# Performance work log

Hardware: AMD Instinct MI355X
Metric: run time of the kernel (lower is better)

Reference implementation:

```python
import jax, jax.numpy as jnp
import numpy as np


def setup_inputs() -> dict:
    key = jax.random.key(0)
    k1, k2, k3 = jax.random.split(key, 3)
    B, Lc, Lq, D = 32, 1024, 128, 1024
    context_features = jax.random.normal(k1, (B, Lc, D), dtype=jnp.float32)
    question_features = jax.random.normal(k2, (B, Lq, D), dtype=jnp.float32)
    # weight of nn.Linear(3*D, 1, bias=False): shape (3*D,), split into w1,w2,w3
    w = jax.random.normal(k3, (3 * D,), dtype=jnp.float32) * (1.0 / np.sqrt(3 * D))
    return {"context_features": context_features, "question_features": question_features, "w": w}


def reference(context_features, question_features, w):
    B, Lc, D = context_features.shape
    Lq = question_features.shape[1]
    w1, w2, w3 = w[:D], w[D:2 * D], w[2 * D:]
    # Trilinear similarity: sim[b,i,j] = w1.c_i + w2.q_j + w3.(c_i*q_j)
    # Decomposed so the (B,Lc,Lq,3D) concat tensor is never materialized.
    sim = (
        jnp.einsum("bcd,d->bc", context_features, w1)[:, :, None]      # [B,Lc,1]
        + jnp.einsum("bqd,d->bq", question_features, w2)[:, None, :]    # [B,1,Lq]
        + jnp.einsum("bcd,bqd->bcq", context_features * w3, question_features)
    )  # [B,Lc,Lq]
    # context-to-question attention
    c2q = jnp.einsum("bcq,bqd->bcd", jax.nn.softmax(sim, axis=2), question_features)
    # question-to-context attention
    b = jax.nn.softmax(jnp.max(sim, axis=2), axis=-1)                   # [B,Lc]
    q2c = jnp.einsum("bc,bcd->bd", b, context_features)                 # [B,D]
    q2c = jnp.broadcast_to(q2c[:, None, :], (B, Lc, D))                 # repeat over Lc
    return (c2q, q2c)
```

## Files before the change

kernel.cpp:

```cpp
#include <hip/hip_runtime.h>
#include <hip/hip_bf16.h>
#include <stdint.h>

#define B_  32
#define LC  1024
#define LQ  128
#define DD  1024
#define CT  64
#define BK  64

typedef __attribute__((ext_vector_type(8))) short short8;
typedef __attribute__((ext_vector_type(4))) float f4;
typedef unsigned short u16;

__device__ __forceinline__ u16 f2bf(float f) {
  __hip_bfloat16 h = __float2bfloat16(f);
  return *reinterpret_cast<u16*>(&h);
}

__device__ __forceinline__ void gld16(const u16* g, void* l) {
  __builtin_amdgcn_global_load_lds(
      (const __attribute__((address_space(1))) unsigned int*)g,
      (__attribute__((address_space(3))) unsigned int*)l,
      16, 0, 0);
}

__global__ __launch_bounds__(256) void k1m(const float* __restrict__ qf,
                                           const float* __restrict__ w,
                                           u16* __restrict__ qw3_bf,
                                           u16* __restrict__ qT_bf,
                                           float* __restrict__ qwpart) {
  __shared__ float w3s[128];
  __shared__ float w2s[128];
  __shared__ __align__(16) u16 ldsq[128][136];
  int blk = blockIdx.x;
  int b = blk >> 3, dt = blk & 7;
  int t = threadIdx.x;
  if (t < 128) { w3s[t] = w[2 * DD + dt * 128 + t]; w2s[t] = w[DD + dt * 128 + t]; }
  __syncthreads();
  {
    int q = t >> 1, half = t & 1;
    const float* src = qf + (size_t)(b * LQ + q) * DD + dt * 128 + half * 64;
    u16* dst = qw3_bf + (size_t)(b * LQ + q) * DD + dt * 128 + half * 64;
    float s2 = 0.f;
    #pragma unroll
    for (int j = 0; j < 8; ++j) {
      float4 a = *(const float4*)(src + j * 8);
      float4 c = *(const float4*)(src + j * 8 + 4);
      float vals[8] = {a.x, a.y, a.z, a.w, c.x, c.y, c.z, c.w};
      u16 u3[8] __attribute__((aligned(16)));
      #pragma unroll
      for (int jj = 0; jj < 8; ++jj) {
        int dl = half * 64 + j * 8 + jj;
        s2 += vals[jj] * w2s[dl];
        u3[jj] = f2bf(vals[jj] * w3s[dl]);
        ldsq[dl][q] = f2bf(vals[jj]);
      }
      *(short8*)(dst + j * 8) = *(short8*)u3;
    }
    s2 += __shfl_xor(s2, 1);
    if (half == 0) qwpart[(size_t)(b * 8 + dt) * LQ + q] = s2;
  }
  __syncthreads();
  {
    int d = t >> 1, qh = (t & 1) * 64;
    u16* gdst = qT_bf + (size_t)b * DD * LQ + (size_t)(dt * 128 + d) * LQ + qh;
    #pragma unroll
    for (int i = 0; i < 8; ++i) {
      short8 v = *(const short8*)(&ldsq[d][qh + i * 8]);
      *(short8*)(gdst + i * 8) = v;
    }
  }
}

__device__ __forceinline__ void stage3(const u16* aqT, int dt,
                                       unsigned char* qbase, int wv, int lane) {
  #pragma unroll
  for (int i = 0; i < 4; ++i) {
    unsigned rel = wv * 4096 + i * 1024 + lane * 16;
    int r = rel >> 8, c = (rel >> 4) & 15, cs = c ^ (r & 7);
    gld16(aqT + (size_t)(dt * 64 + r) * LQ + cs * 8, qbase + wv * 4096 + i * 1024);
  }
}

__global__ __launch_bounds__(256, 3) void kA(const float* __restrict__ ctx,
                                          const u16* __restrict__ qw3_bf,
                                          const u16* __restrict__ qT_bf,
                                          const float* __restrict__ w,
                                          const float* __restrict__ qwpart,
                                          float* __restrict__ c2q,
                                          float* __restrict__ partial,
                                          float* __restrict__ tileM,
                                          float* __restrict__ tileS) {
  __shared__ __align__(16) unsigned char tile[49152];
  __shared__ float cws[CT];
  __shared__ float qws[LQ];
  __shared__ float rm2[2][CT];
  __shared__ float rs2[2][CT];
  __shared__ float rmax[CT];
  __shared__ float rinv[CT];
  __shared__ float wgtl[CT];

  unsigned char* psm = tile + 32768;

  const int tid = threadIdx.x;
  const int bid = blockIdx.x;
  const int blk = (bid & 7) * 64 + (bid >> 3);
  const int b   = blk >> 4;
  const int c0  = (blk & 15) * CT;
  const int lane = tid & 63;
  const int wv   = tid >> 6;
  const int wr   = wv >> 1;
  const int wc   = wv & 1;
  const int l15  = lane & 15;
  const int l4   = lane >> 4;

  if (tid < LQ) {
    float s = 0.f;
    #pragma unroll
    for (int dt = 0; dt < 8; ++dt) s += qwpart[(size_t)(b * 8 + dt) * LQ + tid];
    qws[tid] = s;
  }

  f4 acc[2][4];
  #pragma unroll
  for (int m = 0; m < 2; ++m)
    #pragma unroll
    for (int n = 0; n < 4; ++n) { f4 z = {0.f, 0.f, 0.f, 0.f}; acc[m][n] = z; }

  const float* actx = ctx + (size_t)(b * LC + c0) * DD;
  const u16* aq3  = qw3_bf + (size_t)b * LQ * DD;
  const u16* aqT  = qT_bf + (size_t)b * DD * LQ;

  const int ar  = tid >> 2;
  const int akc = (tid & 3) * 16;

  float va[16];
  float cwp = 0.f;
  const float* w1p = w + akc;

  {
    const float* s = actx + (size_t)ar * DD + akc;
    *(float4*)(va)      = *(const float4*)(s);
    *(float4*)(va + 4)  = *(const float4*)(s + 4);
    *(float4*)(va + 8)  = *(const float4*)(s + 8);
    *(float4*)(va + 12) = *(const float4*)(s + 12);
    #pragma unroll
    for (int i = 0; i < 4; ++i) {
      unsigned rel = wv * 4096 + i * 1024 + lane * 16;
      int r = rel >> 7, c = (rel >> 4) & 7, cs = c ^ (r & 7);
      gld16(aq3 + (size_t)r * DD + cs * 8, tile + 8192 + wv * 4096 + i * 1024);
    }
    #pragma unroll
    for (int j = 0; j < 4; ++j) {
      float4 wv4 = *(const float4*)(w1p + j * 4);
      cwp += va[j * 4 + 0] * wv4.x + va[j * 4 + 1] * wv4.y +
             va[j * 4 + 2] * wv4.z + va[j * 4 + 3] * wv4.w;
    }
    u16 u[16] __attribute__((aligned(16)));
    #pragma unroll
    for (int j = 0; j < 16; ++j) u[j] = f2bf(va[j]);
    int cu = akc >> 3;
    *(short8*)(tile + ar * 128 + ((cu ^ (ar & 7)) << 4))       = *(short8*)u;
    *(short8*)(tile + ar * 128 + (((cu + 1) ^ (ar & 7)) << 4)) = *(short8*)(u + 8);
  }
  __syncthreads();

  for (int t = 0; t < 16; ++t) {
    int cur = t & 1;
    unsigned char* bufc = tile + cur * 24576;
    unsigned char* bufn = tile + (cur ^ 1) * 24576;
    if (t < 15) {
      int k0_ = (t + 1) * BK;
      const float* s = actx + (size_t)ar * DD + k0_ + akc;
      *(float4*)(va)      = *(const float4*)(s);
      *(float4*)(va + 4)  = *(const float4*)(s + 4);
      *(float4*)(va + 8)  = *(const float4*)(s + 8);
      *(float4*)(va + 12) = *(const float4*)(s + 12);
      #pragma unroll
      for (int i = 0; i < 4; ++i) {
        unsigned rel = wv * 4096 + i * 1024 + lane * 16;
        int r = rel >> 7, c = (rel >> 4) & 7, cs = c ^ (r & 7);
        gld16(aq3 + (size_t)r * DD + k0_ + cs * 8, bufn + 8192 + wv * 4096 + i * 1024);
      }
      #pragma unroll
      for (int j = 0; j < 4; ++j) {
        float4 wv4 = *(const float4*)(w1p + k0_ + j * 4);
        cwp += va[j * 4 + 0] * wv4.x + va[j * 4 + 1] * wv4.y +
               va[j * 4 + 2] * wv4.z + va[j * 4 + 3] * wv4.w;
      }
    }
    #pragma unroll
    for (int kk = 0; kk < 2; ++kk) {
      short8 afr[2], bfr[4];
      #pragma unroll
      for (int m = 0; m < 2; ++m) {
        int r = wr * 32 + m * 16 + l15;
        int byte = r * 128 + kk * 64 + l4 * 16;
        byte ^= (r & 7) << 4;
        afr[m] = *(const short8*)(bufc + byte);
      }
      #pragma unroll
      for (int n = 0; n < 4; ++n) {
        int r = wc * 64 + n * 16 + l15;
        int byte = r * 128 + kk * 64 + l4 * 16;
        byte ^= (r & 7) << 4;
        bfr[n] = *(const short8*)(bufc + 8192 + byte);
      }
      #pragma unroll
      for (int m = 0; m < 2; ++m)
        #pragma unroll
        for (int n = 0; n < 4; ++n)
          acc[m][n] = __builtin_amdgcn_mfma_f32_16x16x32_bf16(afr[m], bfr[n], acc[m][n], 0, 0, 0);
    }
    if (t < 15) {
      u16 u[16] __attribute__((aligned(16)));
      #pragma unroll
      for (int j = 0; j < 16; ++j) u[j] = f2bf(va[j]);
      int cu = akc >> 3;
      *(short8*)(bufn + ar * 128 + ((cu ^ (ar & 7)) << 4))       = *(short8*)u;
      *(short8*)(bufn + ar * 128 + (((cu + 1) ^ (ar & 7)) << 4)) = *(short8*)(u + 8);
    }
    __syncthreads();
  }

  cwp += __shfl_xor(cwp, 1);
  cwp += __shfl_xor(cwp, 2);
  if ((lane & 3) == 0) cws[ar] = cwp;
  __syncthreads();

  #pragma unroll
  for (int m = 0; m < 2; ++m) {
    #pragma unroll
    for (int j = 0; j < 4; ++j) {
      int cl = wr * 32 + m * 16 + l4 * 4 + j;
      float mx = -1e30f;
      #pragma unroll
      for (int n = 0; n < 4; ++n) {
        float v = acc[m][n][j] + cws[cl] + qws[wc * 64 + n * 16 + l15];
        acc[m][n][j] = v;
        mx = fmaxf(mx, v);
      }
      #pragma unroll
      for (int off = 1; off < 16; off <<= 1) mx = fmaxf(mx, __shfl_xor(mx, off));
      if (l15 == 0) rm2[wc][cl] = mx;
    }
  }
  __syncthreads();
  if (tid < CT) rmax[tid] = fmaxf(rm2[0][tid], rm2[1][tid]);
  __syncthreads();
  #pragma unroll
  for (int m = 0; m < 2; ++m) {
    #pragma unroll
    for (int j = 0; j < 4; ++j) {
      int cl = wr * 32 + m * 16 + l4 * 4 + j;
      float mx = rmax[cl];
      float s = 0.f;
      #pragma unroll
      for (int n = 0; n < 4; ++n) {
        float p = __expf(acc[m][n][j] - mx);
        s += p;
        int q = wc * 64 + n * 16 + l15;
        int byte = cl * (LQ * 2) + q * 2;
        byte ^= (cl & 7) << 4;
        *(u16*)(psm + byte) = f2bf(p);
      }
      #pragma unroll
      for (int off = 1; off < 16; off <<= 1) s += __shfl_xor(s, off);
      if (l15 == 0) rs2[wc][cl] = s;
    }
  }
  __syncthreads();
  if (tid < CT) {
    rinv[tid] = 1.f / (rs2[0][tid] + rs2[1][tid]);
    float m = rmax[tid];
    float M = m;
    #pragma unroll
    for (int off = 32; off; off >>= 1) M = fmaxf(M, __shfl_xor(M, off));
    float wq = __expf(m - M);
    wgtl[tid] = wq;
    float S = wq;
    #pragma unroll
    for (int off = 32; off; off >>= 1) S += __shfl_xor(S, off);
    if (tid == 0) { tileM[blk] = M; tileS[blk] = S; }
  }
  __syncthreads();

  stage3(aqT, 0, tile, wv, lane);
  __syncthreads();

  float ri[2];
  ri[0] = rinv[wr * 32 + l15];
  ri[1] = rinv[wr * 32 + 16 + l15];

  f4 pacc25 = {0.f, 0.f, 0.f, 0.f};
  const float* pbase = actx + tid * 4;

  for (int dt = 0; dt < 16; ++dt) {
    int cur = dt & 1;
    if (dt < 15) stage3(aqT, dt + 1, tile + (cur ^ 1) * 16384, wv, lane);
    #pragma unroll
    for (int cc = 0; cc < 4; ++cc) {
      int c = dt * 4 + cc;
      pacc25 += wgtl[c] * *(const f4*)(pbase + (size_t)c * DD);
    }
    unsigned char* qbase = tile + cur * 16384;
    f4 pacc[2][2];
    #pragma unroll
    for (int n = 0; n < 2; ++n)
      #pragma unroll
      for (int m = 0; m < 2; ++m) { f4 z = {0.f, 0.f, 0.f, 0.f}; pacc[n][m] = z; }
    #pragma unroll
    for (int kk = 0; kk < 4; ++kk) {
      short8 pa[2], qb[2];
      #pragma unroll
      for (int m = 0; m < 2; ++m) {
        int r = wr * 32 + m * 16 + l15;
        int byte = r * 256 + kk * 64 + l4 * 16;
        byte ^= (r & 7) << 4;
        pa[m] = *(const short8*)(psm + byte);
      }
      #pragma unroll
      for (int n = 0; n < 2; ++n) {
        int dl = wc * 32 + n * 16 + l15;
        int byte = dl * 256 + kk * 64 + l4 * 16;
        byte ^= (dl & 7) << 4;
        qb[n] = *(const short8*)(qbase + byte);
      }
      #pragma unroll
      for (int n = 0; n < 2; ++n)
        #pragma unroll
        for (int m = 0; m < 2; ++m)
          pacc[n][m] = __builtin_amdgcn_mfma_f32_16x16x32_bf16(qb[n], pa[m], pacc[n][m], 0, 0, 0);
    }
    #pragma unroll
    for (int n = 0; n < 2; ++n)
      #pragma unroll
      for (int m = 0; m < 2; ++m) {
        f4 v = pacc[n][m] * ri[m];
        int cl = wr * 32 + m * 16 + l15;
        int dc = wc * 32 + n * 16 + l4 * 4;
        *(f4*)(c2q + (size_t)(b * LC + c0 + cl) * DD + dt * 64 + dc) = v;
      }
    __syncthreads();
  }

  *(f4*)(partial + (size_t)blk * DD + tid * 4) = pacc25;
}

__global__ __launch_bounds__(256) void kQC2(const float* __restrict__ partial,
                                            const float* __restrict__ tileM,
                                            const float* __restrict__ tileS,
                                            float* __restrict__ out2) {
  int blk = blockIdx.x;
  int b = blk >> 5, cb = blk & 31;
  int t = threadIdx.x;
  __shared__ float sc[16];
  __shared__ float dninv;
  if (t < 16) {
    float m = tileM[b * 16 + t];
    float M = m;
    #pragma unroll
    for (int off = 8; off; off >>= 1) M = fmaxf(M, __shfl_xor(M, off));
    float e = __expf(m - M);
    sc[t] = e;
    float d = e * tileS[b * 16 + t];
    #pragma unroll
    for (int off = 8; off; off >>= 1) d += __shfl_xor(d, off);
    if (t == 0) dninv = 1.f / d;
  }
  __syncthreads();
  f4 a = {0.f, 0.f, 0.f, 0.f};
  #pragma unroll
  for (int i = 0; i < 16; ++i) {
    float s = sc[i];
    f4 v = *(const f4*)(partial + (size_t)(b * 16 + i) * DD + t * 4);
    a += s * v;
  }
  a *= dninv;
  float* dst = out2 + ((size_t)b * LC + cb * 32) * DD + t * 4;
  #pragma unroll
  for (int r = 0; r < 32; ++r) *(f4*)(dst + (size_t)r * DD) = a;
}

extern "C" void kernel_launch(void* const* d_in, const int* in_sizes, int n_in,
                              void* d_out, int out_size, void* d_ws, size_t ws_size,
                              hipStream_t stream) {
  (void)in_sizes; (void)n_in; (void)out_size; (void)ws_size;
  const float* ctx = (const float*)d_in[0];
  const float* qf  = (const float*)d_in[1];
  const float* w   = (const float*)d_in[2];
  float* out      = (float*)d_out;
  float* c2q      = out;
  float* q2c_out  = out + (size_t)B_ * LC * DD;

  float* ws     = (float*)d_ws;
  float* qwpart = ws;
  float* tileM  = qwpart + B_ * 8 * LQ;
  float* tileS  = tileM + 512;
  float* part   = tileS + 512;
  u16*   qw3_bf = (u16*)(part + 512 * DD);
  u16*   qT_bf  = qw3_bf + (size_t)B_ * LQ * DD;

  hipLaunchKernelGGL(k1m,  dim3(256),  dim3(256), 0, stream, qf, w, qw3_bf, qT_bf, qwpart);
  hipLaunchKernelGGL(kA,   dim3(512),  dim3(256), 0, stream, ctx, qw3_bf, qT_bf, w, qwpart, c2q, part, tileM, tileS);
  hipLaunchKernelGGL(kQC2, dim3(1024), dim3(256), 0, stream, part, tileM, tileS, q2c_out);
}
```

Measured before the change: 137.6 us.

## Deepen context prefetch to two stages with partial vmcnt barriers in kA

Restructures the phase-1 GEMM loop in kA so context rows are register-prefetched two K-steps ahead, using alternating register buffers. Each step now ends with a custom barrier that waits only until vmcnt drops to 4, so the most recent global loads can stay in flight across the barrier. The w1 vector is staged into shared memory instead of being read from global on every step. Launch bounds drop from 3 to 2 blocks per SM, which allows more registers per thread for the second buffer but lowers occupancy. The hand-set vmcnt count is fragile if the compiler reorders or merges loads.

```diff
diff --git a/kernel.cpp b/kernel.cpp
--- a/kernel.cpp
+++ b/kernel.cpp
@@ -23,6 +23,13 @@
       (const __attribute__((address_space(1))) unsigned int*)g,
       (__attribute__((address_space(3))) unsigned int*)l,
       16, 0, 0);
+}
+
+__device__ __forceinline__ void barrier_vm4() {
+  __builtin_amdgcn_sched_barrier(0);
+  asm volatile("s_waitcnt vmcnt(4) lgkmcnt(0)" ::: "memory");
+  __builtin_amdgcn_s_barrier();
+  __builtin_amdgcn_sched_barrier(0);
 }
 
 __global__ __launch_bounds__(256) void k1m(const float* __restrict__ qf,
@@ -83,7 +90,84 @@
   }
 }
 
-__global__ __launch_bounds__(256, 3) void kA(const float* __restrict__ ctx,
+#define STAGEB_PH1(K0, BUF)                                                    \
+  do {                                                                         \
+    _Pragma("unroll")                                                          \
+    for (int i_ = 0; i_ < 4; ++i_) {                                           \
+      unsigned rel_ = wv * 4096 + i_ * 1024 + lane * 16;                       \
+      int r_ = rel_ >> 7, c_ = (rel_ >> 4) & 7, cs_ = c_ ^ (r_ & 7);           \
+      gld16(aq3 + (size_t)r_ * DD + (K0) + cs_ * 8,                            \
+            (BUF) + 8192 + wv * 4096 + i_ * 1024);                             \
+    }                                                                          \
+  } while (0)
+
+#define LOADCTX_PH1(VA, K0)                                                    \
+  do {                                                                         \
+    const float* s_ = actx + (size_t)ar * DD + (K0) + akc;                     \
+    *(float4*)(VA)      = *(const float4*)(s_);                                \
+    *(float4*)(VA + 4)  = *(const float4*)(s_ + 4);                            \
+    *(float4*)(VA + 8)  = *(const float4*)(s_ + 8);                            \
+    *(float4*)(VA + 12) = *(const float4*)(s_ + 12);                           \
+  } while (0)
+
+#define CWWRITE_PH1(VA, K0, BUF)                                               \
+  do {                                                                         \
+    _Pragma("unroll")                                                          \
+    for (int j_ = 0; j_ < 4; ++j_) {                                           \
+      float4 w4_ = *(const float4*)(&w1s[(K0) + akc + j_ * 4]);                \
+      cwp += (VA)[j_ * 4 + 0] * w4_.x + (VA)[j_ * 4 + 1] * w4_.y +             \
+             (VA)[j_ * 4 + 2] * w4_.z + (VA)[j_ * 4 + 3] * w4_.w;              \
+    }                                                                          \
+    {                                                                          \
+      u16 u_[16] __attribute__((aligned(16)));                                 \
+      _Pragma("unroll")                                                        \
+      for (int j_ = 0; j_ < 16; ++j_) u_[j_] = f2bf((VA)[j_]);                 \
+      int cu_ = akc >> 3;                                                      \
+      *(short8*)((BUF) + ar * 128 + ((cu_ ^ (ar & 7)) << 4)) = *(short8*)u_;   \
+      *(short8*)((BUF) + ar * 128 + (((cu_ + 1) ^ (ar & 7)) << 4)) =           \
+          *(short8*)(u_ + 8);                                                  \
+    }                                                                          \
+  } while (0)
+
+#define MFMA_PH1(BUFC)                                                         \
+  do {                                                                         \
+    _Pragma("unroll")                                                          \
+    for (int kk = 0; kk < 2; ++kk) {                                           \
+      short8 afr[2], bfr[4];                                                   \
+      _Pragma("unroll")                                                        \
+      for (int m_ = 0; m_ < 2; ++m_) {                                         \
+        int r_ = wr * 32 + m_ * 16 + l15;                                      \
+        int byte_ = r_ * 128 + kk * 64 + l4 * 16;                              \
+        byte_ ^= (r_ & 7) << 4;                                                \
+        afr[m_] = *(const short8*)((BUFC) + byte_);                            \
+      }                                                                        \
+      _Pragma("unroll")                                                        \
+      for (int n_ = 0; n_ < 4; ++n_) {                                         \
+        int r_ = wc * 64 + n_ * 16 + l15;                                      \
+        int byte_ = r_ * 128 + kk * 64 + l4 * 16;                              \
+        byte_ ^= (r_ & 7) << 4;                                                \
+        bfr[n_] = *(const short8*)((BUFC) + 8192 + byte_);                     \
+      }                                                                        \
+      _Pragma("unroll")                                                        \
+      for (int m_ = 0; m_ < 2; ++m_)                                           \
+        _Pragma("unroll")                                                      \
+        for (int n_ = 0; n_ < 4; ++n_)                                         \
+          acc[m_][n_] = __builtin_amdgcn_mfma_f32_16x16x32_bf16(               \
+              afr[m_], bfr[n_], acc[m_][n_], 0, 0, 0);                         \
+    }                                                                          \
+  } while (0)
+
+#define PH1_ITER(T, VA_WR, VA_LD, BUFC, BUFN)                                  \
+  do {                                                                         \
+    STAGEB_PH1(((T) + 1) * BK, BUFN);                                          \
+    __builtin_amdgcn_sched_barrier(0);                                         \
+    LOADCTX_PH1(VA_LD, ((T) + 2) * BK);                                        \
+    MFMA_PH1(BUFC);                                                            \
+    CWWRITE_PH1(VA_WR, ((T) + 1) * BK, BUFN);                                  \
+    barrier_vm4();                                                             \
+  } while (0)
+
+__global__ __launch_bounds__(256, 2) void kA(const float* __restrict__ ctx,
                                           const u16* __restrict__ qw3_bf,
                                           const u16* __restrict__ qT_bf,
                                           const float* __restrict__ w,
@@ -93,6 +177,7 @@
                                           float* __restrict__ tileM,
                                           float* __restrict__ tileS) {
   __shared__ __align__(16) unsigned char tile[49152];
+  __shared__ __align__(16) float w1s[DD];
   __shared__ float cws[CT];
   __shared__ float qws[LQ];
   __shared__ float rm2[2][CT];
@@ -115,6 +200,7 @@
   const int l15  = lane & 15;
   const int l4   = lane >> 4;
 
+  *(f4*)(&w1s[tid * 4]) = *(const f4*)(w + tid * 4);
   if (tid < LQ) {
     float s = 0.f;
     #pragma unroll
@@ -135,94 +221,33 @@
   const int ar  = tid >> 2;
   const int akc = (tid & 3) * 16;
 
-  float va[16];
+  float vaA[16], vaB[16];
   float cwp = 0.f;
-  const float* w1p = w + akc;
+
+  __syncthreads();
 
   {
-    const float* s = actx + (size_t)ar * DD + akc;
-    *(float4*)(va)      = *(const float4*)(s);
-    *(float4*)(va + 4)  = *(const float4*)(s + 4);
-    *(float4*)(va + 8)  = *(const float4*)(s + 8);
-    *(float4*)(va + 12) = *(const float4*)(s + 12);
-    #pragma unroll
-    for (int i = 0; i < 4; ++i) {
-      unsigned rel = wv * 4096 + i * 1024 + lane * 16;
-      int r = rel >> 7, c = (rel >> 4) & 7, cs = c ^ (r & 7);
-      gld16(aq3 + (size_t)r * DD + cs * 8, tile + 8192 + wv * 4096 + i * 1024);
-    }
-    #pragma unroll
-    for (int j = 0; j < 4; ++j) {
-      float4 wv4 = *(const float4*)(w1p + j * 4);
-      cwp += va[j * 4 + 0] * wv4.x + va[j * 4 + 1] * wv4.y +
-             va[j * 4 + 2] * wv4.z + va[j * 4 + 3] * wv4.w;
-    }
-    u16 u[16] __attribute__((aligned(16)));
-    #pragma unroll
-    for (int j = 0; j < 16; ++j) u[j] = f2bf(va[j]);
-    int cu = akc >> 3;
-    *(short8*)(tile + ar * 128 + ((cu ^ (ar & 7)) << 4))       = *(short8*)u;
-    *(short8*)(tile + ar * 128 + (((cu + 1) ^ (ar & 7)) << 4)) = *(short8*)(u + 8);
-  }
-  __syncthreads();
-
-  for (int t = 0; t < 16; ++t) {
-    int cur = t & 1;
-    unsigned char* bufc = tile + cur * 24576;
-    unsigned char* bufn = tile + (cur ^ 1) * 24576;
-    if (t < 15) {
-      int k0_ = (t + 1) * BK;
-      const float* s = actx + (size_t)ar * DD + k0_ + akc;
-      *(float4*)(va)      = *(const float4*)(s);
-      *(float4*)(va + 4)  = *(const float4*)(s + 4);
-      *(float4*)(va + 8)  = *(const float4*)(s + 8);
-      *(float4*)(va + 12) = *(const float4*)(s + 12);
-      #pragma unroll
-      for (int i = 0; i < 4; ++i) {
-        unsigned rel = wv * 4096 + i * 1024 + lane * 16;
-        int r = rel >> 7, c = (rel >> 4) & 7, cs = c ^ (r & 7);
-        gld16(aq3 + (size_t)r * DD + k0_ + cs * 8, bufn + 8192 + wv * 4096 + i * 1024);
-      }
-      #pragma unroll
-      for (int j = 0; j < 4; ++j) {
-        float4 wv4 = *(const float4*)(w1p + k0_ + j * 4);
-        cwp += va[j * 4 + 0] * wv4.x + va[j * 4 + 1] * wv4.y +
-               va[j * 4 + 2] * wv4.z + va[j * 4 + 3] * wv4.w;
-      }
-    }
-    #pragma unroll
-    for (int kk = 0; kk < 2; ++kk) {
-      short8 afr[2], bfr[4];
-      #pragma unroll
-      for (int m = 0; m < 2; ++m) {
-        int r = wr * 32 + m * 16 + l15;
-        int byte = r * 128 + kk * 64 + l4 * 16;
-        byte ^= (r & 7) << 4;
-        afr[m] = *(const short8*)(bufc + byte);
-      }
-      #pragma unroll
-      for (int n = 0; n < 4; ++n) {
-        int r = wc * 64 + n * 16 + l15;
-        int byte = r * 128 + kk * 64 + l4 * 16;
-        byte ^= (r & 7) << 4;
-        bfr[n] = *(const short8*)(bufc + 8192 + byte);
-      }
-      #pragma unroll
-      for (int m = 0; m < 2; ++m)
-        #pragma unroll
-        for (int n = 0; n < 4; ++n)
-          acc[m][n] = __builtin_amdgcn_mfma_f32_16x16x32_bf16(afr[m], bfr[n], acc[m][n], 0, 0, 0);
-    }
-    if (t < 15) {
-      u16 u[16] __attribute__((aligned(16)));
-      #pragma unroll
-      for (int j = 0; j < 16; ++j) u[j] = f2bf(va[j]);
-      int cu = akc >> 3;
-      *(short8*)(bufn + ar * 128 + ((cu ^ (ar & 7)) << 4))       = *(short8*)u;
-      *(short8*)(bufn + ar * 128 + (((cu + 1) ^ (ar & 7)) << 4)) = *(short8*)(u + 8);
-    }
+    LOADCTX_PH1(vaA, 0);
+    __builtin_amdgcn_sched_barrier(0);
+    STAGEB_PH1(0, tile);
+    __builtin_amdgcn_sched_barrier(0);
+    CWWRITE_PH1(vaA, 0, tile);
+    LOADCTX_PH1(vaB, BK);
+    barrier_vm4();
+  }
+
+  for (int t2 = 0; t2 < 7; ++t2) {
+    PH1_ITER(2 * t2,     vaB, vaA, tile,         tile + 24576);
+    PH1_ITER(2 * t2 + 1, vaA, vaB, tile + 24576, tile);
+  }
+  {
+    STAGEB_PH1(15 * BK, tile + 24576);
+    MFMA_PH1(tile);
+    CWWRITE_PH1(vaB, 15 * BK, tile + 24576);
     __syncthreads();
   }
+  MFMA_PH1(tile + 24576);
+  __syncthreads();
 
   cwp += __shfl_xor(cwp, 1);
   cwp += __shfl_xor(cwp, 2);
```

New measurement: 136.4 us. No clear change (-0.8%).

## Double kA block to 512 threads with 2x4 wave grid and staged w1

Applied to the files above, without the earlier changes.

Widens the main attention kernel from 4 to 8 waves per block. The sim GEMM and the P·Q GEMM are split over a 2x4 wave grid, so each wave holds half the accumulators. Loads are split finer and the q2c partial sums are reduced across two thread halves through LDS. The w1 weights are cached in shared memory and the cw dot product is moved after the MFMAs. The aim is more latency hiding per CU with lower register pressure per thread, at the cost of more barrier participants and extra LDS use.

```diff
diff --git a/kernel.cpp b/kernel.cpp
--- a/kernel.cpp
+++ b/kernel.cpp
@@ -76,14 +76,14 @@
 __device__ __forceinline__ void stage3(const u16* aqT, int dt,
                                        unsigned char* qbase, int wv, int lane) {
   #pragma unroll
-  for (int i = 0; i < 4; ++i) {
-    unsigned rel = wv * 4096 + i * 1024 + lane * 16;
+  for (int i = 0; i < 2; ++i) {
+    unsigned rel = wv * 2048 + i * 1024 + lane * 16;
     int r = rel >> 8, c = (rel >> 4) & 15, cs = c ^ (r & 7);
-    gld16(aqT + (size_t)(dt * 64 + r) * LQ + cs * 8, qbase + wv * 4096 + i * 1024);
-  }
-}
-
-__global__ __launch_bounds__(256, 3) void kA(const float* __restrict__ ctx,
+    gld16(aqT + (size_t)(dt * 64 + r) * LQ + cs * 8, qbase + wv * 2048 + i * 1024);
+  }
+}
+
+__global__ __launch_bounds__(512, 4) void kA(const float* __restrict__ ctx,
                                           const u16* __restrict__ qw3_bf,
                                           const u16* __restrict__ qT_bf,
                                           const float* __restrict__ w,
@@ -93,10 +93,11 @@
                                           float* __restrict__ tileM,
                                           float* __restrict__ tileS) {
   __shared__ __align__(16) unsigned char tile[49152];
+  __shared__ __align__(16) float w1s[DD];
   __shared__ float cws[CT];
   __shared__ float qws[LQ];
-  __shared__ float rm2[2][CT];
-  __shared__ float rs2[2][CT];
+  __shared__ float rm2[4][CT];
+  __shared__ float rs2[4][CT];
   __shared__ float rmax[CT];
   __shared__ float rinv[CT];
   __shared__ float wgtl[CT];
@@ -110,11 +111,12 @@
   const int c0  = (blk & 15) * CT;
   const int lane = tid & 63;
   const int wv   = tid >> 6;
-  const int wr   = wv >> 1;
-  const int wc   = wv & 1;
+  const int wr   = wv >> 2;
+  const int wc   = wv & 3;
   const int l15  = lane & 15;
   const int l4   = lane >> 4;
 
+  if (tid < 256) *(f4*)(&w1s[tid * 4]) = *(const f4*)(w + tid * 4);
   if (tid < LQ) {
     float s = 0.f;
     #pragma unroll
@@ -122,47 +124,45 @@
     qws[tid] = s;
   }
 
-  f4 acc[2][4];
+  f4 acc[2][2];
   #pragma unroll
   for (int m = 0; m < 2; ++m)
     #pragma unroll
-    for (int n = 0; n < 4; ++n) { f4 z = {0.f, 0.f, 0.f, 0.f}; acc[m][n] = z; }
+    for (int n = 0; n < 2; ++n) { f4 z = {0.f, 0.f, 0.f, 0.f}; acc[m][n] = z; }
 
   const float* actx = ctx + (size_t)(b * LC + c0) * DD;
   const u16* aq3  = qw3_bf + (size_t)b * LQ * DD;
   const u16* aqT  = qT_bf + (size_t)b * DD * LQ;
 
-  const int ar  = tid >> 2;
-  const int akc = (tid & 3) * 16;
-
-  float va[16];
+  const int ar  = tid >> 3;
+  const int akc = (tid & 7) * 8;
+
+  float va[8];
   float cwp = 0.f;
-  const float* w1p = w + akc;
+
+  __syncthreads();
 
   {
     const float* s = actx + (size_t)ar * DD + akc;
-    *(float4*)(va)      = *(const float4*)(s);
-    *(float4*)(va + 4)  = *(const float4*)(s + 4);
-    *(float4*)(va + 8)  = *(const float4*)(s + 8);
-    *(float4*)(va + 12) = *(const float4*)(s + 12);
-    #pragma unroll
-    for (int i = 0; i < 4; ++i) {
-      unsigned rel = wv * 4096 + i * 1024 + lane * 16;
+    *(float4*)(va)     = *(const float4*)(s);
+    *(float4*)(va + 4) = *(const float4*)(s + 4);
+    #pragma unroll
+    for (int i = 0; i < 2; ++i) {
+      unsigned rel = wv * 2048 + i * 1024 + lane * 16;
       int r = rel >> 7, c = (rel >> 4) & 7, cs = c ^ (r & 7);
-      gld16(aq3 + (size_t)r * DD + cs * 8, tile + 8192 + wv * 4096 + i * 1024);
-    }
-    #pragma unroll
-    for (int j = 0; j < 4; ++j) {
-      float4 wv4 = *(const float4*)(w1p + j * 4);
-      cwp += va[j * 4 + 0] * wv4.x + va[j * 4 + 1] * wv4.y +
-             va[j * 4 + 2] * wv4.z + va[j * 4 + 3] * wv4.w;
-    }
-    u16 u[16] __attribute__((aligned(16)));
-    #pragma unroll
-    for (int j = 0; j < 16; ++j) u[j] = f2bf(va[j]);
+      gld16(aq3 + (size_t)r * DD + cs * 8, tile + 8192 + wv * 2048 + i * 1024);
+    }
+    #pragma unroll
+    for (int j = 0; j < 2; ++j) {
+      float4 w4 = *(const float4*)(&w1s[akc + j * 4]);
+      cwp += va[j * 4 + 0] * w4.x + va[j * 4 + 1] * w4.y +
+             va[j * 4 + 2] * w4.z + va[j * 4 + 3] * w4.w;
+    }
+    u16 u[8] __attribute__((aligned(16)));
+    #pragma unroll
+    for (int j = 0; j < 8; ++j) u[j] = f2bf(va[j]);
     int cu = akc >> 3;
-    *(short8*)(tile + ar * 128 + ((cu ^ (ar & 7)) << 4))       = *(short8*)u;
-    *(short8*)(tile + ar * 128 + (((cu + 1) ^ (ar & 7)) << 4)) = *(short8*)(u + 8);
+    *(short8*)(tile + ar * 128 + ((cu ^ (ar & 7)) << 4)) = *(short8*)u;
   }
   __syncthreads();
 
@@ -173,26 +173,18 @@
     if (t < 15) {
       int k0_ = (t + 1) * BK;
       const float* s = actx + (size_t)ar * DD + k0_ + akc;
-      *(float4*)(va)      = *(const float4*)(s);
-      *(float4*)(va + 4)  = *(const float4*)(s + 4);
-      *(float4*)(va + 8)  = *(const float4*)(s + 8);
-      *(float4*)(va + 12) = *(const float4*)(s + 12);
-      #pragma unroll
-      for (int i = 0; i < 4; ++i) {
-        unsigned rel = wv * 4096 + i * 1024 + lane * 16;
+      *(float4*)(va)     = *(const float4*)(s);
+      *(float4*)(va + 4) = *(const float4*)(s + 4);
+      #pragma unroll
+      for (int i = 0; i < 2; ++i) {
+        unsigned rel = wv * 2048 + i * 1024 + lane * 16;
         int r = rel >> 7, c = (rel >> 4) & 7, cs = c ^ (r & 7);
-        gld16(aq3 + (size_t)r * DD + k0_ + cs * 8, bufn + 8192 + wv * 4096 + i * 1024);
-      }
-      #pragma unroll
-      for (int j = 0; j < 4; ++j) {
-        float4 wv4 = *(const float4*)(w1p + k0_ + j * 4);
-        cwp += va[j * 4 + 0] * wv4.x + va[j * 4 + 1] * wv4.y +
-               va[j * 4 + 2] * wv4.z + va[j * 4 + 3] * wv4.w;
+        gld16(aq3 + (size_t)r * DD + k0_ + cs * 8, bufn + 8192 + wv * 2048 + i * 1024);
       }
     }
     #pragma unroll
     for (int kk = 0; kk < 2; ++kk) {
-      short8 afr[2], bfr[4];
+      short8 afr[2], bfr[2];
       #pragma unroll
       for (int m = 0; m < 2; ++m) {
         int r = wr * 32 + m * 16 + l15;
@@ -201,8 +193,8 @@
         afr[m] = *(const short8*)(bufc + byte);
       }
       #pragma unroll
-      for (int n = 0; n < 4; ++n) {
-        int r = wc * 64 + n * 16 + l15;
+      for (int n = 0; n < 2; ++n) {
+        int r = wc * 32 + n * 16 + l15;
         int byte = r * 128 + kk * 64 + l4 * 16;
         byte ^= (r & 7) << 4;
         bfr[n] = *(const short8*)(bufc + 8192 + byte);
@@ -210,23 +202,30 @@
       #pragma unroll
       for (int m = 0; m < 2; ++m)
         #pragma unroll
-        for (int n = 0; n < 4; ++n)
+        for (int n = 0; n < 2; ++n)
           acc[m][n] = __builtin_amdgcn_mfma_f32_16x16x32_bf16(afr[m], bfr[n], acc[m][n], 0, 0, 0);
     }
     if (t < 15) {
-      u16 u[16] __attribute__((aligned(16)));
-      #pragma unroll
-      for (int j = 0; j < 16; ++j) u[j] = f2bf(va[j]);
+      int k0_ = (t + 1) * BK;
+      #pragma unroll
+      for (int j = 0; j < 2; ++j) {
+        float4 w4 = *(const float4*)(&w1s[k0_ + akc + j * 4]);
+        cwp += va[j * 4 + 0] * w4.x + va[j * 4 + 1] * w4.y +
+               va[j * 4 + 2] * w4.z + va[j * 4 + 3] * w4.w;
+      }
+      u16 u[8] __attribute__((aligned(16)));
+      #pragma unroll
+      for (int j = 0; j < 8; ++j) u[j] = f2bf(va[j]);
       int cu = akc >> 3;
-      *(short8*)(bufn + ar * 128 + ((cu ^ (ar & 7)) << 4))       = *(short8*)u;
-      *(short8*)(bufn + ar * 128 + (((cu + 1) ^ (ar & 7)) << 4)) = *(short8*)(u + 8);
+      *(short8*)(bufn + ar * 128 + ((cu ^ (ar & 7)) << 4)) = *(short8*)u;
     }
     __syncthreads();
   }
 
   cwp += __shfl_xor(cwp, 1);
   cwp += __shfl_xor(cwp, 2);
-  if ((lane & 3) == 0) cws[ar] = cwp;
+  cwp += __shfl_xor(cwp, 4);
+  if ((lane & 7) == 0) cws[ar] = cwp;
   __syncthreads();
 
   #pragma unroll
@@ -236,8 +235,8 @@
       int cl = wr * 32 + m * 16 + l4 * 4 + j;
       float mx = -1e30f;
       #pragma unroll
-      for (int n = 0; n < 4; ++n) {
-        float v = acc[m][n][j] + cws[cl] + qws[wc * 64 + n * 16 + l15];
+      for (int n = 0; n < 2; ++n) {
+        float v = acc[m][n][j] + cws[cl] + qws[wc * 32 + n * 16 + l15];
         acc[m][n][j] = v;
         mx = fmaxf(mx, v);
       }
@@ -247,7 +246,8 @@
     }
   }
   __syncthreads();
-  if (tid < CT) rmax[tid] = fmaxf(rm2[0][tid], rm2[1][tid]);
+  if (tid < CT)
+    rmax[tid] = fmaxf(fmaxf(rm2[0][tid], rm2[1][tid]), fmaxf(rm2[2][tid], rm2[3][tid]));
   __syncthreads();
   #pragma unroll
   for (int m = 0; m < 2; ++m) {
@@ -257,10 +257,10 @@
       float mx = rmax[cl];
       float s = 0.f;
       #pragma unroll
-      for (int n = 0; n < 4; ++n) {
+      for (int n = 0; n < 2; ++n) {
         float p = __expf(acc[m][n][j] - mx);
         s += p;
-        int q = wc * 64 + n * 16 + l15;
+        int q = wc * 32 + n * 16 + l15;
         int byte = cl * (LQ * 2) + q * 2;
         byte ^= (cl & 7) << 4;
         *(u16*)(psm + byte) = f2bf(p);
@@ -272,7 +272,7 @@
   }
   __syncthreads();
   if (tid < CT) {
-    rinv[tid] = 1.f / (rs2[0][tid] + rs2[1][tid]);
+    rinv[tid] = 1.f / (rs2[0][tid] + rs2[1][tid] + rs2[2][tid] + rs2[3][tid]);
     float m = rmax[tid];
     float M = m;
     #pragma unroll
@@ -294,25 +294,24 @@
   ri[1] = rinv[wr * 32 + 16 + l15];
 
   f4 pacc25 = {0.f, 0.f, 0.f, 0.f};
-  const float* pbase = actx + tid * 4;
+  const int rh = tid >> 8;
+  const int d4 = (tid & 255) * 4;
+  const float* pbase = actx + d4;
 
   for (int dt = 0; dt < 16; ++dt) {
     int cur = dt & 1;
     if (dt < 15) stage3(aqT, dt + 1, tile + (cur ^ 1) * 16384, wv, lane);
     #pragma unroll
-    for (int cc = 0; cc < 4; ++cc) {
-      int c = dt * 4 + cc;
+    for (int cc = 0; cc < 2; ++cc) {
+      int c = dt * 4 + rh * 2 + cc;
       pacc25 += wgtl[c] * *(const f4*)(pbase + (size_t)c * DD);
     }
     unsigned char* qbase = tile + cur * 16384;
-    f4 pacc[2][2];
-    #pragma unroll
-    for (int n = 0; n < 2; ++n)
-      #pragma unroll
-      for (int m = 0; m < 2; ++m) { f4 z = {0.f, 0.f, 0.f, 0.f}; pacc[n][m] = z; }
+    f4 pacc[2];
+    { f4 z = {0.f, 0.f, 0.f, 0.f}; pacc[0] = z; pacc[1] = z; }
     #pragma unroll
     for (int kk = 0; kk < 4; ++kk) {
-      short8 pa[2], qb[2];
+      short8 pa[2], qb;
       #pragma unroll
       for (int m = 0; m < 2; ++m) {
         int r = wr * 32 + m * 16 + l15;
@@ -320,32 +319,32 @@
         byte ^= (r & 7) << 4;
         pa[m] = *(const short8*)(psm + byte);
       }
-      #pragma unroll
-      for (int n = 0; n < 2; ++n) {
-        int dl = wc * 32 + n * 16 + l15;
+      {
+        int dl = wc * 16 + l15;
         int byte = dl * 256 + kk * 64 + l4 * 16;
         byte ^= (dl & 7) << 4;
-        qb[n] = *(const short8*)(qbase + byte);
-      }
-      #pragma unroll
-      for (int n = 0; n < 2; ++n)
-        #pragma unroll
-        for (int m = 0; m < 2; ++m)
-          pacc[n][m] = __builtin_amdgcn_mfma_f32_16x16x32_bf16(qb[n], pa[m], pacc[n][m], 0, 0, 0);
-    }
-    #pragma unroll
-    for (int n = 0; n < 2; ++n)
-      #pragma unroll
-      for (int m = 0; m < 2; ++m) {
-        f4 v = pacc[n][m] * ri[m];
-        int cl = wr * 32 + m * 16 + l15;
-        int dc = wc * 32 + n * 16 + l4 * 4;
-        *(f4*)(c2q + (size_t)(b * LC + c0 + cl) * DD + dt * 64 + dc) = v;
-      }
+        qb = *(const short8*)(qbase + byte);
+      }
+      #pragma unroll
+      for (int m = 0; m < 2; ++m)
+        pacc[m] = __builtin_amdgcn_mfma_f32_16x16x32_bf16(qb, pa[m], pacc[m], 0, 0, 0);
+    }
+    #pragma unroll
+    for (int m = 0; m < 2; ++m) {
+      f4 v = pacc[m] * ri[m];
+      int cl = wr * 32 + m * 16 + l15;
+      int dc = wc * 16 + l4 * 4;
+      *(f4*)(c2q + (size_t)(b * LC + c0 + cl) * DD + dt * 64 + dc) = v;
+    }
     __syncthreads();
   }
 
-  *(f4*)(partial + (size_t)blk * DD + tid * 4) = pacc25;
+  if (rh == 1) *(f4*)(tile + (tid & 255) * 16) = pacc25;
+  __syncthreads();
+  if (rh == 0) {
+    f4 o = pacc25 + *(const f4*)(tile + tid * 16);
+    *(f4*)(partial + (size_t)blk * DD + d4) = o;
+  }
 }
 
 __global__ __launch_bounds__(256) void kQC2(const float* __restrict__ partial,
@@ -403,6 +402,6 @@
   u16*   qT_bf  = qw3_bf + (size_t)B_ * LQ * DD;
 
   hipLaunchKernelGGL(k1m,  dim3(256),  dim3(256), 0, stream, qf, w, qw3_bf, qT_bf, qwpart);
-  hipLaunchKernelGGL(kA,   dim3(512),  dim3(256), 0, stream, ctx, qw3_bf, qT_bf, w, qwpart, c2q, part, tileM, tileS);
+  hipLaunchKernelGGL(kA,   dim3(512),  dim3(512), 0, stream, ctx, qw3_bf, qT_bf, w, qwpart, c2q, part, tileM, tileS);
   hipLaunchKernelGGL(kQC2, dim3(1024), dim3(256), 0, stream, part, tileM, tileS, q2c_out);
 }
```

New measurement: 141.9 us. 3.2% more time.
